# Performance work log

Measured on AMD Instinct MI355X. Metric: run time of the kernel, lower is better.

Reference implementation:

```python
import jax, jax.numpy as jnp
import numpy as np

NUM_EXPERTS = 8
TOP_K = 2
HIDDEN = 2048
INTER = 5632
TOKENS = 2048
W_SCALE = 0.02  # keep activations in a sane numeric range


def setup_inputs() -> dict:
    key = jax.random.key(0)
    k1, k2, k3, k4, k5 = jax.random.split(key, 5)
    hidden_states = jax.random.normal(k1, (TOKENS, HIDDEN), dtype=jnp.float32)
    router_logits = jax.random.normal(k2, (TOKENS, NUM_EXPERTS), dtype=jnp.float32)
    w1 = jax.random.normal(k3, (NUM_EXPERTS, INTER, HIDDEN), dtype=jnp.float32) * W_SCALE
    w3 = jax.random.normal(k4, (NUM_EXPERTS, INTER, HIDDEN), dtype=jnp.float32) * W_SCALE
    w2 = jax.random.normal(k5, (NUM_EXPERTS, HIDDEN, INTER), dtype=jnp.float32) * W_SCALE
    return {"hidden_states": hidden_states, "router_logits": router_logits,
            "w1": w1, "w3": w3, "w2": w2}


def reference(hidden_states, router_logits, w1, w3, w2):
    # Routing: top-k over softmax(logits), renormalized (standard TopK routing).
    T = hidden_states.shape[0]
    probs = jax.nn.softmax(router_logits.astype(jnp.float32), axis=-1)  # [T, E]
    top_w, top_idx = jax.lax.top_k(probs, TOP_K)                        # [T, K]
    top_w = top_w / jnp.sum(top_w, axis=-1, keepdims=True)
    # Per-token per-expert combine weight (0 for unselected experts): [T, E]
    comb = jnp.zeros((T, NUM_EXPERTS), dtype=jnp.float32)
    comb = comb.at[jnp.arange(T)[:, None], top_idx].add(top_w)
    x = hidden_states.astype(jnp.float32)  # accumulation in fp32 as in reference
    out = jnp.zeros_like(x)
    for e in range(NUM_EXPERTS):  # fixed small expert count; data dims vectorized
        gate = x @ w1[e].T                     # [T, I]
        up = x @ w3[e].T                       # [T, I]
        y = (jax.nn.silu(gate) * up) @ w2[e].T  # [T, H]
        out = out + comb[:, e:e + 1] * y
    return out
```

## Files before the change

kernel.cpp:

```cpp
#include <hip/hip_runtime.h>
#include <hip/hip_bf16.h>
#include <cstdint>
#include <cstddef>

#define NTOK 2048
#define HID  2048
#define NINT 5632
#define NEXP 8

typedef __attribute__((ext_vector_type(8))) short short8;
typedef __attribute__((ext_vector_type(4))) float f32x4;
typedef __attribute__((ext_vector_type(4))) int   int4v;
typedef __attribute__((ext_vector_type(4))) float fl4;

__device__ __forceinline__ unsigned short f2bf(float f) {
    union { float f; unsigned int u; } v; v.f = f;
    unsigned int r = (v.u + 0x7fffu + ((v.u >> 16) & 1u)) >> 16;
    return (unsigned short)r;
}

__global__ void zero_kernel(float* __restrict__ out, int* __restrict__ meta) {
    int idx = blockIdx.x * blockDim.x + threadIdx.x;
    fl4 z = {0.f, 0.f, 0.f, 0.f};
    ((fl4*)out)[idx] = z;
    if (blockIdx.x == 0 && threadIdx.x < 16) meta[threadIdx.x] = 0;
}

__device__ __forceinline__ void top2_route(const float* __restrict__ lg, int t,
                                           int& e0, int& e1, float& w0, float& w1) {
    float l[NEXP];
#pragma unroll
    for (int e = 0; e < NEXP; ++e) l[e] = lg[t * NEXP + e];
    e0 = 0; float b0l = l[0];
#pragma unroll
    for (int e = 1; e < NEXP; ++e) if (l[e] > b0l) { b0l = l[e]; e0 = e; }
    e1 = (e0 == 0) ? 1 : 0; float b1l = l[e1];
#pragma unroll
    for (int e = 0; e < NEXP; ++e) {
        if (e == e0) continue;
        if (l[e] > b1l) { b1l = l[e]; e1 = e; }
    }
    float m = b0l;
    float p0 = __expf(b0l - m), p1 = __expf(b1l - m);
    float inv = 1.f / (p0 + p1);
    w0 = p0 * inv; w1 = p1 * inv;
}

__global__ void route_count(const float* __restrict__ logits, int* __restrict__ meta) {
    int t = blockIdx.x * blockDim.x + threadIdx.x;
    int e0, e1; float w0, w1;
    top2_route(logits, t, e0, e1, w0, w1);
    atomicAdd(&meta[e0], 1);
    atomicAdd(&meta[e1], 1);
}

__global__ void scan_kernel(int* __restrict__ meta) {
    if (threadIdx.x == 0 && blockIdx.x == 0) {
        int s = 0;
#pragma unroll
        for (int e = 0; e < NEXP; ++e) { meta[16 + e] = s; s += meta[e]; }
        meta[16 + NEXP] = s;
    }
}

__global__ void route_assign(const float* __restrict__ logits, int* __restrict__ meta,
                             int* __restrict__ rowTok, float* __restrict__ rowW) {
    int t = blockIdx.x * blockDim.x + threadIdx.x;
    int e0, e1; float w0, w1;
    top2_route(logits, t, e0, e1, w0, w1);
    int p0 = atomicAdd(&meta[8 + e0], 1);
    int s0 = meta[16 + e0] + p0;
    rowTok[s0] = t; rowW[s0] = w0;
    int p1 = atomicAdd(&meta[8 + e1], 1);
    int s1 = meta[16 + e1] + p1;
    rowTok[s1] = t; rowW[s1] = w1;
}

__global__ void gather_x(const float* __restrict__ x, const int* __restrict__ rowTok,
                         unsigned short* __restrict__ xg) {
    int slot = blockIdx.x;
    int tok = rowTok[slot];
    int c = threadIdx.x;
    const fl4* src = (const fl4*)(x + (size_t)tok * HID);
    fl4 a = src[c * 2], b = src[c * 2 + 1];
    short8 v;
    v[0] = (short)f2bf(a[0]); v[1] = (short)f2bf(a[1]); v[2] = (short)f2bf(a[2]); v[3] = (short)f2bf(a[3]);
    v[4] = (short)f2bf(b[0]); v[5] = (short)f2bf(b[1]); v[6] = (short)f2bf(b[2]); v[7] = (short)f2bf(b[3]);
    *(short8*)(xg + (size_t)slot * HID + c * 8) = v;
}

__global__ __launch_bounds__(512, 2) void gemm1_kernel(
        const unsigned short* __restrict__ xg,
        const float* __restrict__ w1, const float* __restrict__ w3,
        const int* __restrict__ meta, unsigned short* __restrict__ act) {
    int it = blockIdx.x;
    int e  = blockIdx.y;
    int ch = blockIdx.z;
    int r0 = meta[16 + e];
    int Ne = meta[16 + e + 1] - r0;
    int cb = ch * 256;
    if (cb >= Ne) return;

    __shared__ __align__(16) short As[256][72];
    __shared__ __align__(16) short Bs[128][72];

    int tid = threadIdx.x;
    int lane = tid & 63, w = tid >> 6;

    f32x4 acc[2][8];
#pragma unroll
    for (int m = 0; m < 2; ++m)
#pragma unroll
        for (int n = 0; n < 8; ++n) acc[m][n] = (f32x4){0.f, 0.f, 0.f, 0.f};

    int ar = tid >> 1, ah = (tid & 1) * 32;
    int asrow = cb + ar;
    const unsigned short* aptr = xg + (size_t)(r0 + (asrow < Ne ? asrow : 0)) * HID + ah;
    int br = tid >> 2, bq = (tid & 3) * 16;
    const float* wsrc = (br < 64)
        ? (w1 + ((size_t)e * NINT + (size_t)it * 64 + br) * HID + bq)
        : (w3 + ((size_t)e * NINT + (size_t)it * 64 + (br - 64)) * HID + bq);

    for (int k0 = 0; k0 < HID; k0 += 64) {
        int4v av[4];
#pragma unroll
        for (int i = 0; i < 4; ++i) av[i] = *(const int4v*)(aptr + k0 + i * 8);
        fl4 bv[4];
#pragma unroll
        for (int i = 0; i < 4; ++i) bv[i] = *(const fl4*)(wsrc + k0 + i * 4);
        short8 c0, c1;
#pragma unroll
        for (int i = 0; i < 4; ++i) { c0[i] = (short)f2bf(bv[0][i]); c0[i + 4] = (short)f2bf(bv[1][i]); }
#pragma unroll
        for (int i = 0; i < 4; ++i) { c1[i] = (short)f2bf(bv[2][i]); c1[i + 4] = (short)f2bf(bv[3][i]); }

#pragma unroll
        for (int i = 0; i < 4; ++i) *(int4v*)&As[ar][ah + i * 8] = av[i];
        *(short8*)&Bs[br][bq] = c0;
        *(short8*)&Bs[br][bq + 8] = c1;
        __syncthreads();

#pragma unroll
        for (int kk = 0; kk < 64; kk += 32) {
            int ko = kk + (lane >> 4) * 8;
            short8 a0 = *(const short8*)&As[w * 32 + (lane & 15)][ko];
            short8 a1 = *(const short8*)&As[w * 32 + 16 + (lane & 15)][ko];
#pragma unroll
            for (int n = 0; n < 8; ++n) {
                short8 b = *(const short8*)&Bs[n * 16 + (lane & 15)][ko];
                acc[0][n] = __builtin_amdgcn_mfma_f32_16x16x32_bf16(a0, b, acc[0][n], 0, 0, 0);
                acc[1][n] = __builtin_amdgcn_mfma_f32_16x16x32_bf16(a1, b, acc[1][n], 0, 0, 0);
            }
        }
        __syncthreads();
    }

    int rq = lane >> 4, cl = lane & 15;
#pragma unroll
    for (int m = 0; m < 2; ++m) {
#pragma unroll
        for (int n = 0; n < 4; ++n) {
            f32x4 g = acc[m][n], u = acc[m][n + 4];
#pragma unroll
            for (int j = 0; j < 4; ++j) {
                int lr = w * 32 + m * 16 + rq * 4 + j;
                int srow = cb + lr;
                if (srow < Ne) {
                    float gv = g[j];
                    float y = gv / (1.f + __expf(-gv)) * u[j];
                    act[(size_t)(r0 + srow) * NINT + it * 64 + n * 16 + cl] = f2bf(y);
                }
            }
        }
    }
}

__global__ __launch_bounds__(512, 2) void gemm2_kernel(
        const unsigned short* __restrict__ act, const float* __restrict__ w2,
        const int* __restrict__ meta, const int* __restrict__ rowTok,
        const float* __restrict__ rowW, float* __restrict__ out) {
    int ht = blockIdx.x;
    int e  = blockIdx.y;
    int ch = blockIdx.z;
    int r0 = meta[16 + e];
    int Ne = meta[16 + e + 1] - r0;
    int cb = ch * 256;
    if (cb >= Ne) return;

    __shared__ __align__(16) short As[256][72];
    __shared__ __align__(16) short Bs[64][72];

    int tid = threadIdx.x;
    int lane = tid & 63, w = tid >> 6;

    f32x4 acc[2][4];
#pragma unroll
    for (int m = 0; m < 2; ++m)
#pragma unroll
        for (int n = 0; n < 4; ++n) acc[m][n] = (f32x4){0.f, 0.f, 0.f, 0.f};

    int ar = tid >> 1, ah = (tid & 1) * 32;
    int asrow = cb + ar;
    const unsigned short* aptr = act + (size_t)(r0 + (asrow < Ne ? asrow : 0)) * NINT + ah;
    int br = tid >> 3, bq = (tid & 7) * 8;
    const float* bptr = w2 + ((size_t)e * HID + (size_t)ht * 64 + br) * NINT + bq;

    for (int k0 = 0; k0 < NINT; k0 += 64) {
        int4v av[4];
#pragma unroll
        for (int i = 0; i < 4; ++i) av[i] = *(const int4v*)(aptr + k0 + i * 8);
        fl4 bv0 = *(const fl4*)(bptr + k0);
        fl4 bv1 = *(const fl4*)(bptr + k0 + 4);
        short8 bc;
#pragma unroll
        for (int i = 0; i < 4; ++i) { bc[i] = (short)f2bf(bv0[i]); bc[i + 4] = (short)f2bf(bv1[i]); }

#pragma unroll
        for (int i = 0; i < 4; ++i) *(int4v*)&As[ar][ah + i * 8] = av[i];
        *(short8*)&Bs[br][bq] = bc;
        __syncthreads();

#pragma unroll
        for (int kk = 0; kk < 64; kk += 32) {
            int ko = kk + (lane >> 4) * 8;
            short8 a0 = *(const short8*)&As[w * 32 + (lane & 15)][ko];
            short8 a1 = *(const short8*)&As[w * 32 + 16 + (lane & 15)][ko];
#pragma unroll
            for (int n = 0; n < 4; ++n) {
                short8 b = *(const short8*)&Bs[n * 16 + (lane & 15)][ko];
                acc[0][n] = __builtin_amdgcn_mfma_f32_16x16x32_bf16(a0, b, acc[0][n], 0, 0, 0);
                acc[1][n] = __builtin_amdgcn_mfma_f32_16x16x32_bf16(a1, b, acc[1][n], 0, 0, 0);
            }
        }
        __syncthreads();
    }

    int rq = lane >> 4, cl = lane & 15;
#pragma unroll
    for (int m = 0; m < 2; ++m) {
#pragma unroll
        for (int j = 0; j < 4; ++j) {
            int lr = w * 32 + m * 16 + rq * 4 + j;
            int srow = cb + lr;
            if (srow < Ne) {
                int slot = r0 + srow;
                int tok = rowTok[slot];
                float sw = rowW[slot];
#pragma unroll
                for (int n = 0; n < 4; ++n) {
                    atomicAdd(&out[(size_t)tok * HID + ht * 64 + n * 16 + cl], acc[m][n][j] * sw);
                }
            }
        }
    }
}

extern "C" void kernel_launch(void* const* d_in, const int* in_sizes, int n_in,
                              void* d_out, int out_size, void* d_ws, size_t ws_size,
                              hipStream_t stream) {
    const float* x      = (const float*)d_in[0];
    const float* logits = (const float*)d_in[1];
    const float* w1     = (const float*)d_in[2];
    const float* w3     = (const float*)d_in[3];
    const float* w2     = (const float*)d_in[4];
    float* out = (float*)d_out;

    char* ws = (char*)d_ws;
    int*   meta   = (int*)ws;
    int*   rowTok = (int*)(ws + 512);
    float* rowW   = (float*)(ws + 512 + 16384);
    unsigned short* xg  = (unsigned short*)(ws + (1u << 20));
    unsigned short* act = (unsigned short*)(ws + (18u << 20));

    zero_kernel<<<4096, 256, 0, stream>>>(out, meta);
    route_count<<<8, 256, 0, stream>>>(logits, meta);
    scan_kernel<<<1, 1, 0, stream>>>(meta);
    route_assign<<<8, 256, 0, stream>>>(logits, meta, rowTok, rowW);
    gather_x<<<4096, 256, 0, stream>>>(x, rowTok, xg);
    gemm1_kernel<<<dim3(88, 8, 8), 512, 0, stream>>>(xg, w1, w3, meta, act);
    gemm2_kernel<<<dim3(32, 8, 8), 512, 0, stream>>>(act, w2, meta, rowTok, rowW, out);
}
```

Baseline: 741.3 us.

## Register double-buffer global loads in both GEMMs and halve gemm1 N-tile

Both expert GEMMs now prefetch the next K-slice of activations and fp32 weights into registers while the current slice is in shared memory and feeding MFMAs, hiding global load latency behind compute. Gemm1's intermediate tile shrinks from 64 to 32 columns per block (doubling the grid to 176 tiles), which reduces accumulator registers and shared memory per block. The trade-off is more blocks re-reading the same gathered activation rows, and extra registers held for the prefetch buffers.

```diff
diff --git a/kernel.cpp b/kernel.cpp
--- a/kernel.cpp
+++ b/kernel.cpp
@@ -102,65 +102,68 @@
     if (cb >= Ne) return;
 
     __shared__ __align__(16) short As[256][72];
-    __shared__ __align__(16) short Bs[128][72];
+    __shared__ __align__(16) short Bs[64][72];
 
     int tid = threadIdx.x;
     int lane = tid & 63, w = tid >> 6;
 
-    f32x4 acc[2][8];
+    f32x4 acc[2][4];
 #pragma unroll
     for (int m = 0; m < 2; ++m)
 #pragma unroll
-        for (int n = 0; n < 8; ++n) acc[m][n] = (f32x4){0.f, 0.f, 0.f, 0.f};
+        for (int n = 0; n < 4; ++n) acc[m][n] = (f32x4){0.f, 0.f, 0.f, 0.f};
 
     int ar = tid >> 1, ah = (tid & 1) * 32;
     int asrow = cb + ar;
     const unsigned short* aptr = xg + (size_t)(r0 + (asrow < Ne ? asrow : 0)) * HID + ah;
-    int br = tid >> 2, bq = (tid & 3) * 16;
-    const float* wsrc = (br < 64)
-        ? (w1 + ((size_t)e * NINT + (size_t)it * 64 + br) * HID + bq)
-        : (w3 + ((size_t)e * NINT + (size_t)it * 64 + (br - 64)) * HID + bq);
-
-    for (int k0 = 0; k0 < HID; k0 += 64) {
-        int4v av[4];
-#pragma unroll
-        for (int i = 0; i < 4; ++i) av[i] = *(const int4v*)(aptr + k0 + i * 8);
-        fl4 bv[4];
-#pragma unroll
-        for (int i = 0; i < 4; ++i) bv[i] = *(const fl4*)(wsrc + k0 + i * 4);
-        short8 c0, c1;
-#pragma unroll
-        for (int i = 0; i < 4; ++i) { c0[i] = (short)f2bf(bv[0][i]); c0[i + 4] = (short)f2bf(bv[1][i]); }
-#pragma unroll
-        for (int i = 0; i < 4; ++i) { c1[i] = (short)f2bf(bv[2][i]); c1[i + 4] = (short)f2bf(bv[3][i]); }
-
-#pragma unroll
-        for (int i = 0; i < 4; ++i) *(int4v*)&As[ar][ah + i * 8] = av[i];
-        *(short8*)&Bs[br][bq] = c0;
-        *(short8*)&Bs[br][bq + 8] = c1;
-        __syncthreads();
-
-#pragma unroll
-        for (int kk = 0; kk < 64; kk += 32) {
-            int ko = kk + (lane >> 4) * 8;
-            short8 a0 = *(const short8*)&As[w * 32 + (lane & 15)][ko];
-            short8 a1 = *(const short8*)&As[w * 32 + 16 + (lane & 15)][ko];
-#pragma unroll
-            for (int n = 0; n < 8; ++n) {
-                short8 b = *(const short8*)&Bs[n * 16 + (lane & 15)][ko];
-                acc[0][n] = __builtin_amdgcn_mfma_f32_16x16x32_bf16(a0, b, acc[0][n], 0, 0, 0);
-                acc[1][n] = __builtin_amdgcn_mfma_f32_16x16x32_bf16(a1, b, acc[1][n], 0, 0, 0);
-            }
-        }
-        __syncthreads();
-    }
+    int br = tid >> 3, bq = (tid & 7) * 8;
+    const float* wsrc = (br < 32)
+        ? (w1 + ((size_t)e * NINT + (size_t)it * 32 + br) * HID + bq)
+        : (w3 + ((size_t)e * NINT + (size_t)it * 32 + (br - 32)) * HID + bq);
+
+    int4v ra[2][4];
+    fl4   rb[2][2];
+
+#define G1_LOAD(S, K0) do { \
+        _Pragma("unroll") for (int i = 0; i < 4; ++i) ra[S][i] = *(const int4v*)(aptr + (K0) + i * 8); \
+        _Pragma("unroll") for (int i = 0; i < 2; ++i) rb[S][i] = *(const fl4*)(wsrc + (K0) + i * 4); \
+    } while (0)
+
+#define G1_SC(S) do { \
+        short8 bc; \
+        _Pragma("unroll") for (int i = 0; i < 4; ++i) { \
+            bc[i] = (short)f2bf(rb[S][0][i]); bc[i + 4] = (short)f2bf(rb[S][1][i]); } \
+        __syncthreads(); \
+        _Pragma("unroll") for (int i = 0; i < 4; ++i) *(int4v*)&As[ar][ah + i * 8] = ra[S][i]; \
+        *(short8*)&Bs[br][bq] = bc; \
+        __syncthreads(); \
+        _Pragma("unroll") for (int kk = 0; kk < 64; kk += 32) { \
+            int ko = kk + (lane >> 4) * 8; \
+            short8 a0 = *(const short8*)&As[w * 32 + (lane & 15)][ko]; \
+            short8 a1 = *(const short8*)&As[w * 32 + 16 + (lane & 15)][ko]; \
+            _Pragma("unroll") for (int n = 0; n < 4; ++n) { \
+                short8 b = *(const short8*)&Bs[n * 16 + (lane & 15)][ko]; \
+                acc[0][n] = __builtin_amdgcn_mfma_f32_16x16x32_bf16(a0, b, acc[0][n], 0, 0, 0); \
+                acc[1][n] = __builtin_amdgcn_mfma_f32_16x16x32_bf16(a1, b, acc[1][n], 0, 0, 0); } } \
+    } while (0)
+
+    G1_LOAD(0, 0);
+#pragma unroll 1
+    for (int k0 = 0; k0 < HID; k0 += 128) {
+        G1_LOAD(1, k0 + 64);
+        G1_SC(0);
+        if (k0 + 128 < HID) G1_LOAD(0, k0 + 128);
+        G1_SC(1);
+    }
+#undef G1_LOAD
+#undef G1_SC
 
     int rq = lane >> 4, cl = lane & 15;
 #pragma unroll
     for (int m = 0; m < 2; ++m) {
 #pragma unroll
-        for (int n = 0; n < 4; ++n) {
-            f32x4 g = acc[m][n], u = acc[m][n + 4];
+        for (int n = 0; n < 2; ++n) {
+            f32x4 g = acc[m][n], u = acc[m][n + 2];
 #pragma unroll
             for (int j = 0; j < 4; ++j) {
                 int lr = w * 32 + m * 16 + rq * 4 + j;
@@ -168,7 +171,7 @@
                 if (srow < Ne) {
                     float gv = g[j];
                     float y = gv / (1.f + __expf(-gv)) * u[j];
-                    act[(size_t)(r0 + srow) * NINT + it * 64 + n * 16 + cl] = f2bf(y);
+                    act[(size_t)(r0 + srow) * NINT + it * 32 + n * 16 + cl] = f2bf(y);
                 }
             }
         }
@@ -205,35 +208,42 @@
     int br = tid >> 3, bq = (tid & 7) * 8;
     const float* bptr = w2 + ((size_t)e * HID + (size_t)ht * 64 + br) * NINT + bq;
 
-    for (int k0 = 0; k0 < NINT; k0 += 64) {
-        int4v av[4];
-#pragma unroll
-        for (int i = 0; i < 4; ++i) av[i] = *(const int4v*)(aptr + k0 + i * 8);
-        fl4 bv0 = *(const fl4*)(bptr + k0);
-        fl4 bv1 = *(const fl4*)(bptr + k0 + 4);
-        short8 bc;
-#pragma unroll
-        for (int i = 0; i < 4; ++i) { bc[i] = (short)f2bf(bv0[i]); bc[i + 4] = (short)f2bf(bv1[i]); }
-
-#pragma unroll
-        for (int i = 0; i < 4; ++i) *(int4v*)&As[ar][ah + i * 8] = av[i];
-        *(short8*)&Bs[br][bq] = bc;
-        __syncthreads();
-
-#pragma unroll
-        for (int kk = 0; kk < 64; kk += 32) {
-            int ko = kk + (lane >> 4) * 8;
-            short8 a0 = *(const short8*)&As[w * 32 + (lane & 15)][ko];
-            short8 a1 = *(const short8*)&As[w * 32 + 16 + (lane & 15)][ko];
-#pragma unroll
-            for (int n = 0; n < 4; ++n) {
-                short8 b = *(const short8*)&Bs[n * 16 + (lane & 15)][ko];
-                acc[0][n] = __builtin_amdgcn_mfma_f32_16x16x32_bf16(a0, b, acc[0][n], 0, 0, 0);
-                acc[1][n] = __builtin_amdgcn_mfma_f32_16x16x32_bf16(a1, b, acc[1][n], 0, 0, 0);
-            }
-        }
-        __syncthreads();
-    }
+    int4v ra[2][4];
+    fl4   rb[2][2];
+
+#define G2_LOAD(S, K0) do { \
+        _Pragma("unroll") for (int i = 0; i < 4; ++i) ra[S][i] = *(const int4v*)(aptr + (K0) + i * 8); \
+        _Pragma("unroll") for (int i = 0; i < 2; ++i) rb[S][i] = *(const fl4*)(bptr + (K0) + i * 4); \
+    } while (0)
+
+#define G2_SC(S) do { \
+        short8 bc; \
+        _Pragma("unroll") for (int i = 0; i < 4; ++i) { \
+            bc[i] = (short)f2bf(rb[S][0][i]); bc[i + 4] = (short)f2bf(rb[S][1][i]); } \
+        __syncthreads(); \
+        _Pragma("unroll") for (int i = 0; i < 4; ++i) *(int4v*)&As[ar][ah + i * 8] = ra[S][i]; \
+        *(short8*)&Bs[br][bq] = bc; \
+        __syncthreads(); \
+        _Pragma("unroll") for (int kk = 0; kk < 64; kk += 32) { \
+            int ko = kk + (lane >> 4) * 8; \
+            short8 a0 = *(const short8*)&As[w * 32 + (lane & 15)][ko]; \
+            short8 a1 = *(const short8*)&As[w * 32 + 16 + (lane & 15)][ko]; \
+            _Pragma("unroll") for (int n = 0; n < 4; ++n) { \
+                short8 b = *(const short8*)&Bs[n * 16 + (lane & 15)][ko]; \
+                acc[0][n] = __builtin_amdgcn_mfma_f32_16x16x32_bf16(a0, b, acc[0][n], 0, 0, 0); \
+                acc[1][n] = __builtin_amdgcn_mfma_f32_16x16x32_bf16(a1, b, acc[1][n], 0, 0, 0); } } \
+    } while (0)
+
+    G2_LOAD(0, 0);
+#pragma unroll 1
+    for (int k0 = 0; k0 < NINT; k0 += 128) {
+        G2_LOAD(1, k0 + 64);
+        G2_SC(0);
+        if (k0 + 128 < NINT) G2_LOAD(0, k0 + 128);
+        G2_SC(1);
+    }
+#undef G2_LOAD
+#undef G2_SC
 
     int rq = lane >> 4, cl = lane & 15;
 #pragma unroll
@@ -277,6 +287,6 @@
     scan_kernel<<<1, 1, 0, stream>>>(meta);
     route_assign<<<8, 256, 0, stream>>>(logits, meta, rowTok, rowW);
     gather_x<<<4096, 256, 0, stream>>>(x, rowTok, xg);
-    gemm1_kernel<<<dim3(88, 8, 8), 512, 0, stream>>>(xg, w1, w3, meta, act);
+    gemm1_kernel<<<dim3(176, 8, 8), 512, 0, stream>>>(xg, w1, w3, meta, act);
     gemm2_kernel<<<dim3(32, 8, 8), 512, 0, stream>>>(act, w2, meta, rowTok, rowW, out);
 }
```

Result: slower. 931.8 us (+25.7%).

## Drop LDS staging in MoE GEMMs, load MFMA operands directly with register prefetch

Applied to the files above, without the earlier changes.

Both expert GEMMs stop staging tiles through shared memory. Each wave now loads its A and B MFMA fragments straight from global memory into registers and prefetches the next k-step while the current one computes. Blocks cover 128-row chunks assigned through a compact list across experts (find_chunk), replacing the padded 3D grid of mostly early-exiting blocks. gemm2 also widens its N tile to 128. This removes LDS traffic and __syncthreads, and fewer launched blocks do nothing. In exchange, weights are re-read from global memory by every wave rather than shared across the block, which leans on L2 hit rates and uncoalesced row-strided loads.

```diff
diff --git a/kernel.cpp b/kernel.cpp
--- a/kernel.cpp
+++ b/kernel.cpp
@@ -10,7 +10,6 @@
 
 typedef __attribute__((ext_vector_type(8))) short short8;
 typedef __attribute__((ext_vector_type(4))) float f32x4;
-typedef __attribute__((ext_vector_type(4))) int   int4v;
 typedef __attribute__((ext_vector_type(4))) float fl4;
 
 __device__ __forceinline__ unsigned short f2bf(float f) {
@@ -89,167 +88,159 @@
     *(short8*)(xg + (size_t)slot * HID + c * 8) = v;
 }
 
-__global__ __launch_bounds__(512, 2) void gemm1_kernel(
+__device__ __forceinline__ bool find_chunk(const int* __restrict__ meta, int yc,
+                                           int& e, int& ch, int& r0, int& Ne) {
+    e = -1; ch = 0; int accb = 0;
+#pragma unroll
+    for (int i = 0; i < NEXP; ++i) {
+        int nei = meta[17 + i] - meta[16 + i];
+        int cnt = (nei + 127) >> 7;
+        if (e < 0 && yc < accb + cnt) { e = i; ch = yc - accb; }
+        accb += cnt;
+    }
+    if (e < 0) return false;
+    r0 = meta[16 + e]; Ne = meta[17 + e] - r0;
+    return true;
+}
+
+__global__ __launch_bounds__(256, 2) void gemm1_kernel(
         const unsigned short* __restrict__ xg,
         const float* __restrict__ w1, const float* __restrict__ w3,
         const int* __restrict__ meta, unsigned short* __restrict__ act) {
     int it = blockIdx.x;
-    int e  = blockIdx.y;
-    int ch = blockIdx.z;
-    int r0 = meta[16 + e];
-    int Ne = meta[16 + e + 1] - r0;
-    int cb = ch * 256;
-    if (cb >= Ne) return;
-
-    __shared__ __align__(16) short As[256][72];
-    __shared__ __align__(16) short Bs[128][72];
-
-    int tid = threadIdx.x;
-    int lane = tid & 63, w = tid >> 6;
+    int e, ch, r0, Ne;
+    if (!find_chunk(meta, blockIdx.y, e, ch, r0, Ne)) return;
+
+    int lane = threadIdx.x & 63, w = threadIdx.x >> 6;
+    int cl = lane & 15, kq = lane >> 4;
+    int rowb = ch * 128 + w * 32;
+
+    int ra0 = rowb + cl;      if (ra0 > Ne - 1) ra0 = Ne - 1;
+    int ra1 = rowb + 16 + cl; if (ra1 > Ne - 1) ra1 = Ne - 1;
+    const unsigned short* a0p = xg + (size_t)(r0 + ra0) * HID + kq * 8;
+    const unsigned short* a1p = xg + (size_t)(r0 + ra1) * HID + kq * 8;
+
+    const float* bp[8];
+#pragma unroll
+    for (int f = 0; f < 4; ++f) {
+        bp[f]     = w1 + ((size_t)e * NINT + it * 64 + f * 16 + cl) * HID + kq * 8;
+        bp[f + 4] = w3 + ((size_t)e * NINT + it * 64 + f * 16 + cl) * HID + kq * 8;
+    }
 
     f32x4 acc[2][8];
 #pragma unroll
     for (int m = 0; m < 2; ++m)
 #pragma unroll
-        for (int n = 0; n < 8; ++n) acc[m][n] = (f32x4){0.f, 0.f, 0.f, 0.f};
-
-    int ar = tid >> 1, ah = (tid & 1) * 32;
-    int asrow = cb + ar;
-    const unsigned short* aptr = xg + (size_t)(r0 + (asrow < Ne ? asrow : 0)) * HID + ah;
-    int br = tid >> 2, bq = (tid & 3) * 16;
-    const float* wsrc = (br < 64)
-        ? (w1 + ((size_t)e * NINT + (size_t)it * 64 + br) * HID + bq)
-        : (w3 + ((size_t)e * NINT + (size_t)it * 64 + (br - 64)) * HID + bq);
-
-    for (int k0 = 0; k0 < HID; k0 += 64) {
-        int4v av[4];
-#pragma unroll
-        for (int i = 0; i < 4; ++i) av[i] = *(const int4v*)(aptr + k0 + i * 8);
-        fl4 bv[4];
-#pragma unroll
-        for (int i = 0; i < 4; ++i) bv[i] = *(const fl4*)(wsrc + k0 + i * 4);
-        short8 c0, c1;
-#pragma unroll
-        for (int i = 0; i < 4; ++i) { c0[i] = (short)f2bf(bv[0][i]); c0[i + 4] = (short)f2bf(bv[1][i]); }
-#pragma unroll
-        for (int i = 0; i < 4; ++i) { c1[i] = (short)f2bf(bv[2][i]); c1[i + 4] = (short)f2bf(bv[3][i]); }
-
-#pragma unroll
-        for (int i = 0; i < 4; ++i) *(int4v*)&As[ar][ah + i * 8] = av[i];
-        *(short8*)&Bs[br][bq] = c0;
-        *(short8*)&Bs[br][bq + 8] = c1;
-        __syncthreads();
-
-#pragma unroll
-        for (int kk = 0; kk < 64; kk += 32) {
-            int ko = kk + (lane >> 4) * 8;
-            short8 a0 = *(const short8*)&As[w * 32 + (lane & 15)][ko];
-            short8 a1 = *(const short8*)&As[w * 32 + 16 + (lane & 15)][ko];
-#pragma unroll
-            for (int n = 0; n < 8; ++n) {
-                short8 b = *(const short8*)&Bs[n * 16 + (lane & 15)][ko];
-                acc[0][n] = __builtin_amdgcn_mfma_f32_16x16x32_bf16(a0, b, acc[0][n], 0, 0, 0);
-                acc[1][n] = __builtin_amdgcn_mfma_f32_16x16x32_bf16(a1, b, acc[1][n], 0, 0, 0);
-            }
-        }
-        __syncthreads();
-    }
-
-    int rq = lane >> 4, cl = lane & 15;
+        for (int f = 0; f < 8; ++f) acc[m][f] = (f32x4){0.f, 0.f, 0.f, 0.f};
+
+    fl4 b0[8], b1[8];
+#pragma unroll
+    for (int f = 0; f < 8; ++f) { b0[f] = *(const fl4*)(bp[f]); b1[f] = *(const fl4*)(bp[f] + 4); }
+    short8 a0 = *(const short8*)a0p;
+    short8 a1 = *(const short8*)a1p;
+
+#pragma unroll 1
+    for (int k0 = 0; k0 < HID; k0 += 32) {
+        __builtin_amdgcn_s_barrier();
+        int kn = (k0 + 32 < HID) ? (k0 + 32) : 0;
+        short8 a0n = *(const short8*)(a0p + kn);
+        short8 a1n = *(const short8*)(a1p + kn);
+#pragma unroll
+        for (int f = 0; f < 8; ++f) {
+            short8 bb;
+#pragma unroll
+            for (int i = 0; i < 4; ++i) { bb[i] = (short)f2bf(b0[f][i]); bb[i + 4] = (short)f2bf(b1[f][i]); }
+            b0[f] = *(const fl4*)(bp[f] + kn);
+            b1[f] = *(const fl4*)(bp[f] + kn + 4);
+            acc[0][f] = __builtin_amdgcn_mfma_f32_16x16x32_bf16(a0, bb, acc[0][f], 0, 0, 0);
+            acc[1][f] = __builtin_amdgcn_mfma_f32_16x16x32_bf16(a1, bb, acc[1][f], 0, 0, 0);
+        }
+        a0 = a0n; a1 = a1n;
+    }
+
 #pragma unroll
     for (int m = 0; m < 2; ++m) {
 #pragma unroll
-        for (int n = 0; n < 4; ++n) {
-            f32x4 g = acc[m][n], u = acc[m][n + 4];
+        for (int f = 0; f < 4; ++f) {
+            f32x4 g = acc[m][f], u = acc[m][f + 4];
 #pragma unroll
             for (int j = 0; j < 4; ++j) {
-                int lr = w * 32 + m * 16 + rq * 4 + j;
-                int srow = cb + lr;
-                if (srow < Ne) {
+                int lr = rowb + m * 16 + kq * 4 + j;
+                if (lr < Ne) {
                     float gv = g[j];
                     float y = gv / (1.f + __expf(-gv)) * u[j];
-                    act[(size_t)(r0 + srow) * NINT + it * 64 + n * 16 + cl] = f2bf(y);
+                    act[(size_t)(r0 + lr) * NINT + it * 64 + f * 16 + cl] = f2bf(y);
                 }
             }
         }
     }
 }
 
-__global__ __launch_bounds__(512, 2) void gemm2_kernel(
+__global__ __launch_bounds__(256, 2) void gemm2_kernel(
         const unsigned short* __restrict__ act, const float* __restrict__ w2,
         const int* __restrict__ meta, const int* __restrict__ rowTok,
         const float* __restrict__ rowW, float* __restrict__ out) {
     int ht = blockIdx.x;
-    int e  = blockIdx.y;
-    int ch = blockIdx.z;
-    int r0 = meta[16 + e];
-    int Ne = meta[16 + e + 1] - r0;
-    int cb = ch * 256;
-    if (cb >= Ne) return;
-
-    __shared__ __align__(16) short As[256][72];
-    __shared__ __align__(16) short Bs[64][72];
-
-    int tid = threadIdx.x;
-    int lane = tid & 63, w = tid >> 6;
-
-    f32x4 acc[2][4];
+    int e, ch, r0, Ne;
+    if (!find_chunk(meta, blockIdx.y, e, ch, r0, Ne)) return;
+
+    int lane = threadIdx.x & 63, w = threadIdx.x >> 6;
+    int cl = lane & 15, kq = lane >> 4;
+    int rowb = ch * 128 + w * 32;
+
+    int ra0 = rowb + cl;      if (ra0 > Ne - 1) ra0 = Ne - 1;
+    int ra1 = rowb + 16 + cl; if (ra1 > Ne - 1) ra1 = Ne - 1;
+    const unsigned short* a0p = act + (size_t)(r0 + ra0) * NINT + kq * 8;
+    const unsigned short* a1p = act + (size_t)(r0 + ra1) * NINT + kq * 8;
+
+    const float* bp[8];
+#pragma unroll
+    for (int f = 0; f < 8; ++f)
+        bp[f] = w2 + ((size_t)e * HID + ht * 128 + f * 16 + cl) * NINT + kq * 8;
+
+    f32x4 acc[2][8];
 #pragma unroll
     for (int m = 0; m < 2; ++m)
 #pragma unroll
-        for (int n = 0; n < 4; ++n) acc[m][n] = (f32x4){0.f, 0.f, 0.f, 0.f};
-
-    int ar = tid >> 1, ah = (tid & 1) * 32;
-    int asrow = cb + ar;
-    const unsigned short* aptr = act + (size_t)(r0 + (asrow < Ne ? asrow : 0)) * NINT + ah;
-    int br = tid >> 3, bq = (tid & 7) * 8;
-    const float* bptr = w2 + ((size_t)e * HID + (size_t)ht * 64 + br) * NINT + bq;
-
-    for (int k0 = 0; k0 < NINT; k0 += 64) {
-        int4v av[4];
-#pragma unroll
-        for (int i = 0; i < 4; ++i) av[i] = *(const int4v*)(aptr + k0 + i * 8);
-        fl4 bv0 = *(const fl4*)(bptr + k0);
-        fl4 bv1 = *(const fl4*)(bptr + k0 + 4);
-        short8 bc;
-#pragma unroll
-        for (int i = 0; i < 4; ++i) { bc[i] = (short)f2bf(bv0[i]); bc[i + 4] = (short)f2bf(bv1[i]); }
-
-#pragma unroll
-        for (int i = 0; i < 4; ++i) *(int4v*)&As[ar][ah + i * 8] = av[i];
-        *(short8*)&Bs[br][bq] = bc;
-        __syncthreads();
-
-#pragma unroll
-        for (int kk = 0; kk < 64; kk += 32) {
-            int ko = kk + (lane >> 4) * 8;
-            short8 a0 = *(const short8*)&As[w * 32 + (lane & 15)][ko];
-            short8 a1 = *(const short8*)&As[w * 32 + 16 + (lane & 15)][ko];
-#pragma unroll
-            for (int n = 0; n < 4; ++n) {
-                short8 b = *(const short8*)&Bs[n * 16 + (lane & 15)][ko];
-                acc[0][n] = __builtin_amdgcn_mfma_f32_16x16x32_bf16(a0, b, acc[0][n], 0, 0, 0);
-                acc[1][n] = __builtin_amdgcn_mfma_f32_16x16x32_bf16(a1, b, acc[1][n], 0, 0, 0);
-            }
-        }
-        __syncthreads();
-    }
-
-    int rq = lane >> 4, cl = lane & 15;
+        for (int f = 0; f < 8; ++f) acc[m][f] = (f32x4){0.f, 0.f, 0.f, 0.f};
+
+    fl4 b0[8], b1[8];
+#pragma unroll
+    for (int f = 0; f < 8; ++f) { b0[f] = *(const fl4*)(bp[f]); b1[f] = *(const fl4*)(bp[f] + 4); }
+    short8 a0 = *(const short8*)a0p;
+    short8 a1 = *(const short8*)a1p;
+
+#pragma unroll 1
+    for (int k0 = 0; k0 < NINT; k0 += 32) {
+        __builtin_amdgcn_s_barrier();
+        int kn = (k0 + 32 < NINT) ? (k0 + 32) : 0;
+        short8 a0n = *(const short8*)(a0p + kn);
+        short8 a1n = *(const short8*)(a1p + kn);
+#pragma unroll
+        for (int f = 0; f < 8; ++f) {
+            short8 bb;
+#pragma unroll
+            for (int i = 0; i < 4; ++i) { bb[i] = (short)f2bf(b0[f][i]); bb[i + 4] = (short)f2bf(b1[f][i]); }
+            b0[f] = *(const fl4*)(bp[f] + kn);
+            b1[f] = *(const fl4*)(bp[f] + kn + 4);
+            acc[0][f] = __builtin_amdgcn_mfma_f32_16x16x32_bf16(a0, bb, acc[0][f], 0, 0, 0);
+            acc[1][f] = __builtin_amdgcn_mfma_f32_16x16x32_bf16(a1, bb, acc[1][f], 0, 0, 0);
+        }
+        a0 = a0n; a1 = a1n;
+    }
+
 #pragma unroll
     for (int m = 0; m < 2; ++m) {
 #pragma unroll
         for (int j = 0; j < 4; ++j) {
-            int lr = w * 32 + m * 16 + rq * 4 + j;
-            int srow = cb + lr;
-            if (srow < Ne) {
-                int slot = r0 + srow;
+            int lr = rowb + m * 16 + kq * 4 + j;
+            if (lr < Ne) {
+                int slot = r0 + lr;
                 int tok = rowTok[slot];
                 float sw = rowW[slot];
 #pragma unroll
-                for (int n = 0; n < 4; ++n) {
-                    atomicAdd(&out[(size_t)tok * HID + ht * 64 + n * 16 + cl], acc[m][n][j] * sw);
-                }
+                for (int f = 0; f < 8; ++f)
+                    atomicAdd(&out[(size_t)tok * HID + ht * 128 + f * 16 + cl], acc[m][f][j] * sw);
             }
         }
     }
@@ -277,6 +268,6 @@
     scan_kernel<<<1, 1, 0, stream>>>(meta);
     route_assign<<<8, 256, 0, stream>>>(logits, meta, rowTok, rowW);
     gather_x<<<4096, 256, 0, stream>>>(x, rowTok, xg);
-    gemm1_kernel<<<dim3(88, 8, 8), 512, 0, stream>>>(xg, w1, w3, meta, act);
-    gemm2_kernel<<<dim3(32, 8, 8), 512, 0, stream>>>(act, w2, meta, rowTok, rowW, out);
-}
+    gemm1_kernel<<<dim3(88, 40), 256, 0, stream>>>(xg, w1, w3, meta, act);
+    gemm2_kernel<<<dim3(16, 40), 256, 0, stream>>>(act, w2, meta, rowTok, rowW, out);
+}
```

New measurement: 2.853 ms. +284.9%, slower.

## Shrink GEMM tiles, swizzle LDS, reorder grid for weight reuse

Applied to the files above, without the earlier changes.

Both expert GEMMs now use 256-thread blocks with 128-row token tiles and narrower weight tiles (32 intermediate columns for gate/up, 32 hidden columns for down). The grid is reordered so token chunks vary fastest, letting blocks that share a weight tile run together and reuse it from cache. LDS uses an XOR swizzle instead of padding to avoid bank conflicts, the fp32-to-bf16 conversion uses packed intrinsics, and the register-staged loads are issued before the first barrier. The smaller tiles aim for more blocks and better occupancy, but they lower MFMA work per LDS load and double the fp32 weight reads per output.

```diff
diff --git a/kernel.cpp b/kernel.cpp
--- a/kernel.cpp
+++ b/kernel.cpp
@@ -11,12 +11,19 @@
 typedef __attribute__((ext_vector_type(8))) short short8;
 typedef __attribute__((ext_vector_type(4))) float f32x4;
 typedef __attribute__((ext_vector_type(4))) int   int4v;
+typedef __attribute__((ext_vector_type(2))) unsigned int uint2v;
 typedef __attribute__((ext_vector_type(4))) float fl4;
 
 __device__ __forceinline__ unsigned short f2bf(float f) {
     union { float f; unsigned int u; } v; v.f = f;
     unsigned int r = (v.u + 0x7fffu + ((v.u >> 16) & 1u)) >> 16;
     return (unsigned short)r;
+}
+
+__device__ __forceinline__ unsigned int pk2(float x, float y) {
+    __hip_bfloat162 h = __float22bfloat162_rn(make_float2(x, y));
+    union { __hip_bfloat162 h; unsigned int u; } c; c.h = h;
+    return c.u;
 }
 
 __global__ void zero_kernel(float* __restrict__ out, int* __restrict__ meta) {
@@ -89,167 +96,199 @@
     *(short8*)(xg + (size_t)slot * HID + c * 8) = v;
 }
 
-__global__ __launch_bounds__(512, 2) void gemm1_kernel(
+__global__ __launch_bounds__(256, 4) void gemm1_kernel(
         const unsigned short* __restrict__ xg,
         const float* __restrict__ w1, const float* __restrict__ w3,
         const int* __restrict__ meta, unsigned short* __restrict__ act) {
-    int it = blockIdx.x;
-    int e  = blockIdx.y;
-    int ch = blockIdx.z;
-    int r0 = meta[16 + e];
-    int Ne = meta[16 + e + 1] - r0;
-    int cb = ch * 256;
+    const int ch = blockIdx.x;
+    const int it = blockIdx.y;
+    const int e  = blockIdx.z;
+    const int r0 = meta[16 + e];
+    const int Ne = meta[17 + e] - r0;
+    const int cb = ch * 128;
     if (cb >= Ne) return;
 
-    __shared__ __align__(16) short As[256][72];
-    __shared__ __align__(16) short Bs[128][72];
-
-    int tid = threadIdx.x;
-    int lane = tid & 63, w = tid >> 6;
-
-    f32x4 acc[2][8];
-#pragma unroll
-    for (int m = 0; m < 2; ++m)
-#pragma unroll
-        for (int n = 0; n < 8; ++n) acc[m][n] = (f32x4){0.f, 0.f, 0.f, 0.f};
-
-    int ar = tid >> 1, ah = (tid & 1) * 32;
-    int asrow = cb + ar;
-    const unsigned short* aptr = xg + (size_t)(r0 + (asrow < Ne ? asrow : 0)) * HID + ah;
-    int br = tid >> 2, bq = (tid & 3) * 16;
-    const float* wsrc = (br < 64)
-        ? (w1 + ((size_t)e * NINT + (size_t)it * 64 + br) * HID + bq)
-        : (w3 + ((size_t)e * NINT + (size_t)it * 64 + (br - 64)) * HID + bq);
-
+    __shared__ __align__(16) short As[128][64];
+    __shared__ __align__(16) short Bs[64][64];
+
+    const int tid = threadIdx.x;
+    const int wv = tid >> 6, l = tid & 63;
+    const int cl = l & 15, kq = l >> 4;
+
+    const unsigned short* agp[4];
+    short* awr[4];
+    {
+        const int slot = tid & 7;
+#pragma unroll
+        for (int j = 0; j < 4; ++j) {
+            int row = (tid >> 3) + j * 32;
+            int gr = cb + row; if (gr > Ne - 1) gr = Ne - 1;
+            agp[j] = xg + (size_t)(r0 + gr) * HID + slot * 8;
+            awr[j] = &As[row][(slot ^ (row & 7)) * 8];
+        }
+    }
+    const int brow = tid >> 2, bq = tid & 3;
+    const float* bgp = ((brow < 32)
+        ? (w1 + ((size_t)e * NINT + (size_t)it * 32 + brow) * HID)
+        : (w3 + ((size_t)e * NINT + (size_t)it * 32 + (brow - 32)) * HID)) + bq * 4;
+    unsigned int* bwr[4];
+#pragma unroll
+    for (int j2 = 0; j2 < 4; ++j2) {
+        int s = 2 * j2 + (bq >> 1);
+        bwr[j2] = (unsigned int*)&Bs[brow][(s ^ (brow & 7)) * 8 + (bq & 1) * 4];
+    }
+
+    f32x4 acc[2][4];
+#pragma unroll
+    for (int rf = 0; rf < 2; ++rf)
+#pragma unroll
+        for (int cf = 0; cf < 4; ++cf) acc[rf][cf] = (f32x4){0.f, 0.f, 0.f, 0.f};
+
+#pragma unroll 1
     for (int k0 = 0; k0 < HID; k0 += 64) {
-        int4v av[4];
-#pragma unroll
-        for (int i = 0; i < 4; ++i) av[i] = *(const int4v*)(aptr + k0 + i * 8);
-        fl4 bv[4];
-#pragma unroll
-        for (int i = 0; i < 4; ++i) bv[i] = *(const fl4*)(wsrc + k0 + i * 4);
-        short8 c0, c1;
-#pragma unroll
-        for (int i = 0; i < 4; ++i) { c0[i] = (short)f2bf(bv[0][i]); c0[i + 4] = (short)f2bf(bv[1][i]); }
-#pragma unroll
-        for (int i = 0; i < 4; ++i) { c1[i] = (short)f2bf(bv[2][i]); c1[i + 4] = (short)f2bf(bv[3][i]); }
-
-#pragma unroll
-        for (int i = 0; i < 4; ++i) *(int4v*)&As[ar][ah + i * 8] = av[i];
-        *(short8*)&Bs[br][bq] = c0;
-        *(short8*)&Bs[br][bq + 8] = c1;
+        int4v ra[4];
+#pragma unroll
+        for (int j = 0; j < 4; ++j) ra[j] = *(const int4v*)(agp[j] + k0);
+        fl4 rb[4];
+#pragma unroll
+        for (int j2 = 0; j2 < 4; ++j2) rb[j2] = *(const fl4*)(bgp + k0 + 16 * j2);
+        uint2v bw[4];
+#pragma unroll
+        for (int j2 = 0; j2 < 4; ++j2) {
+            bw[j2][0] = pk2(rb[j2][0], rb[j2][1]);
+            bw[j2][1] = pk2(rb[j2][2], rb[j2][3]);
+        }
         __syncthreads();
-
-#pragma unroll
-        for (int kk = 0; kk < 64; kk += 32) {
-            int ko = kk + (lane >> 4) * 8;
-            short8 a0 = *(const short8*)&As[w * 32 + (lane & 15)][ko];
-            short8 a1 = *(const short8*)&As[w * 32 + 16 + (lane & 15)][ko];
-#pragma unroll
-            for (int n = 0; n < 8; ++n) {
-                short8 b = *(const short8*)&Bs[n * 16 + (lane & 15)][ko];
-                acc[0][n] = __builtin_amdgcn_mfma_f32_16x16x32_bf16(a0, b, acc[0][n], 0, 0, 0);
-                acc[1][n] = __builtin_amdgcn_mfma_f32_16x16x32_bf16(a1, b, acc[1][n], 0, 0, 0);
+#pragma unroll
+        for (int j = 0; j < 4; ++j) *(int4v*)awr[j] = ra[j];
+#pragma unroll
+        for (int j2 = 0; j2 < 4; ++j2) *(uint2v*)bwr[j2] = bw[j2];
+        __syncthreads();
+#pragma unroll
+        for (int kk = 0; kk < 2; ++kk) {
+            const int sx = ((kk * 4 + kq) ^ (cl & 7)) * 8;
+            short8 af0 = *(const short8*)&As[wv * 32 + cl][sx];
+            short8 af1 = *(const short8*)&As[wv * 32 + 16 + cl][sx];
+#pragma unroll
+            for (int cf = 0; cf < 4; ++cf) {
+                short8 bfm = *(const short8*)&Bs[cf * 16 + cl][sx];
+                acc[0][cf] = __builtin_amdgcn_mfma_f32_16x16x32_bf16(af0, bfm, acc[0][cf], 0, 0, 0);
+                acc[1][cf] = __builtin_amdgcn_mfma_f32_16x16x32_bf16(af1, bfm, acc[1][cf], 0, 0, 0);
             }
         }
-        __syncthreads();
-    }
-
-    int rq = lane >> 4, cl = lane & 15;
-#pragma unroll
-    for (int m = 0; m < 2; ++m) {
-#pragma unroll
-        for (int n = 0; n < 4; ++n) {
-            f32x4 g = acc[m][n], u = acc[m][n + 4];
+    }
+
+#pragma unroll
+    for (int rf = 0; rf < 2; ++rf) {
+#pragma unroll
+        for (int cf = 0; cf < 2; ++cf) {
+            f32x4 g = acc[rf][cf], u = acc[rf][cf + 2];
 #pragma unroll
             for (int j = 0; j < 4; ++j) {
-                int lr = w * 32 + m * 16 + rq * 4 + j;
-                int srow = cb + lr;
-                if (srow < Ne) {
+                int r = cb + wv * 32 + rf * 16 + kq * 4 + j;
+                if (r < Ne) {
                     float gv = g[j];
                     float y = gv / (1.f + __expf(-gv)) * u[j];
-                    act[(size_t)(r0 + srow) * NINT + it * 64 + n * 16 + cl] = f2bf(y);
+                    act[(size_t)(r0 + r) * NINT + (size_t)it * 32 + cf * 16 + cl] = f2bf(y);
                 }
             }
         }
     }
 }
 
-__global__ __launch_bounds__(512, 2) void gemm2_kernel(
+__global__ __launch_bounds__(256, 4) void gemm2_kernel(
         const unsigned short* __restrict__ act, const float* __restrict__ w2,
         const int* __restrict__ meta, const int* __restrict__ rowTok,
         const float* __restrict__ rowW, float* __restrict__ out) {
-    int ht = blockIdx.x;
-    int e  = blockIdx.y;
-    int ch = blockIdx.z;
-    int r0 = meta[16 + e];
-    int Ne = meta[16 + e + 1] - r0;
-    int cb = ch * 256;
+    const int ch = blockIdx.x;
+    const int ht = blockIdx.y;
+    const int e  = blockIdx.z;
+    const int r0 = meta[16 + e];
+    const int Ne = meta[17 + e] - r0;
+    const int cb = ch * 128;
     if (cb >= Ne) return;
 
-    __shared__ __align__(16) short As[256][72];
-    __shared__ __align__(16) short Bs[64][72];
-
-    int tid = threadIdx.x;
-    int lane = tid & 63, w = tid >> 6;
-
-    f32x4 acc[2][4];
-#pragma unroll
-    for (int m = 0; m < 2; ++m)
-#pragma unroll
-        for (int n = 0; n < 4; ++n) acc[m][n] = (f32x4){0.f, 0.f, 0.f, 0.f};
-
-    int ar = tid >> 1, ah = (tid & 1) * 32;
-    int asrow = cb + ar;
-    const unsigned short* aptr = act + (size_t)(r0 + (asrow < Ne ? asrow : 0)) * NINT + ah;
-    int br = tid >> 3, bq = (tid & 7) * 8;
-    const float* bptr = w2 + ((size_t)e * HID + (size_t)ht * 64 + br) * NINT + bq;
-
+    __shared__ __align__(16) short As[128][64];
+    __shared__ __align__(16) short Bs[32][64];
+
+    const int tid = threadIdx.x;
+    const int wv = tid >> 6, l = tid & 63;
+    const int cl = l & 15, kq = l >> 4;
+
+    const unsigned short* agp[4];
+    short* awr[4];
+    {
+        const int slot = tid & 7;
+#pragma unroll
+        for (int j = 0; j < 4; ++j) {
+            int row = (tid >> 3) + j * 32;
+            int gr = cb + row; if (gr > Ne - 1) gr = Ne - 1;
+            agp[j] = act + (size_t)(r0 + gr) * NINT + slot * 8;
+            awr[j] = &As[row][(slot ^ (row & 7)) * 8];
+        }
+    }
+    const int brow = tid >> 3, bq = tid & 7;
+    const float* bgp = w2 + ((size_t)e * HID + (size_t)ht * 32 + brow) * NINT + bq * 4;
+    unsigned int* bwr[2];
+#pragma unroll
+    for (int j2 = 0; j2 < 2; ++j2) {
+        int s = 4 * j2 + (bq >> 1);
+        bwr[j2] = (unsigned int*)&Bs[brow][(s ^ (brow & 7)) * 8 + (bq & 1) * 4];
+    }
+
+    f32x4 acc[2][2];
+#pragma unroll
+    for (int rf = 0; rf < 2; ++rf)
+#pragma unroll
+        for (int cf = 0; cf < 2; ++cf) acc[rf][cf] = (f32x4){0.f, 0.f, 0.f, 0.f};
+
+#pragma unroll 1
     for (int k0 = 0; k0 < NINT; k0 += 64) {
-        int4v av[4];
-#pragma unroll
-        for (int i = 0; i < 4; ++i) av[i] = *(const int4v*)(aptr + k0 + i * 8);
-        fl4 bv0 = *(const fl4*)(bptr + k0);
-        fl4 bv1 = *(const fl4*)(bptr + k0 + 4);
-        short8 bc;
-#pragma unroll
-        for (int i = 0; i < 4; ++i) { bc[i] = (short)f2bf(bv0[i]); bc[i + 4] = (short)f2bf(bv1[i]); }
-
-#pragma unroll
-        for (int i = 0; i < 4; ++i) *(int4v*)&As[ar][ah + i * 8] = av[i];
-        *(short8*)&Bs[br][bq] = bc;
+        int4v ra[4];
+#pragma unroll
+        for (int j = 0; j < 4; ++j) ra[j] = *(const int4v*)(agp[j] + k0);
+        fl4 rb[2];
+#pragma unroll
+        for (int j2 = 0; j2 < 2; ++j2) rb[j2] = *(const fl4*)(bgp + k0 + 32 * j2);
+        uint2v bw[2];
+#pragma unroll
+        for (int j2 = 0; j2 < 2; ++j2) {
+            bw[j2][0] = pk2(rb[j2][0], rb[j2][1]);
+            bw[j2][1] = pk2(rb[j2][2], rb[j2][3]);
+        }
         __syncthreads();
-
-#pragma unroll
-        for (int kk = 0; kk < 64; kk += 32) {
-            int ko = kk + (lane >> 4) * 8;
-            short8 a0 = *(const short8*)&As[w * 32 + (lane & 15)][ko];
-            short8 a1 = *(const short8*)&As[w * 32 + 16 + (lane & 15)][ko];
-#pragma unroll
-            for (int n = 0; n < 4; ++n) {
-                short8 b = *(const short8*)&Bs[n * 16 + (lane & 15)][ko];
-                acc[0][n] = __builtin_amdgcn_mfma_f32_16x16x32_bf16(a0, b, acc[0][n], 0, 0, 0);
-                acc[1][n] = __builtin_amdgcn_mfma_f32_16x16x32_bf16(a1, b, acc[1][n], 0, 0, 0);
+#pragma unroll
+        for (int j = 0; j < 4; ++j) *(int4v*)awr[j] = ra[j];
+#pragma unroll
+        for (int j2 = 0; j2 < 2; ++j2) *(uint2v*)bwr[j2] = bw[j2];
+        __syncthreads();
+#pragma unroll
+        for (int kk = 0; kk < 2; ++kk) {
+            const int sx = ((kk * 4 + kq) ^ (cl & 7)) * 8;
+            short8 af0 = *(const short8*)&As[wv * 32 + cl][sx];
+            short8 af1 = *(const short8*)&As[wv * 32 + 16 + cl][sx];
+#pragma unroll
+            for (int cf = 0; cf < 2; ++cf) {
+                short8 bfm = *(const short8*)&Bs[cf * 16 + cl][sx];
+                acc[0][cf] = __builtin_amdgcn_mfma_f32_16x16x32_bf16(af0, bfm, acc[0][cf], 0, 0, 0);
+                acc[1][cf] = __builtin_amdgcn_mfma_f32_16x16x32_bf16(af1, bfm, acc[1][cf], 0, 0, 0);
             }
         }
-        __syncthreads();
-    }
-
-    int rq = lane >> 4, cl = lane & 15;
-#pragma unroll
-    for (int m = 0; m < 2; ++m) {
+    }
+
+#pragma unroll
+    for (int rf = 0; rf < 2; ++rf) {
 #pragma unroll
         for (int j = 0; j < 4; ++j) {
-            int lr = w * 32 + m * 16 + rq * 4 + j;
-            int srow = cb + lr;
-            if (srow < Ne) {
-                int slot = r0 + srow;
+            int r = cb + wv * 32 + rf * 16 + kq * 4 + j;
+            if (r < Ne) {
+                int slot = r0 + r;
                 int tok = rowTok[slot];
                 float sw = rowW[slot];
 #pragma unroll
-                for (int n = 0; n < 4; ++n) {
-                    atomicAdd(&out[(size_t)tok * HID + ht * 64 + n * 16 + cl], acc[m][n][j] * sw);
-                }
+                for (int cf = 0; cf < 2; ++cf)
+                    atomicAdd(&out[(size_t)tok * HID + (size_t)ht * 32 + cf * 16 + cl],
+                              acc[rf][cf][j] * sw);
             }
         }
     }
@@ -277,6 +316,6 @@
     scan_kernel<<<1, 1, 0, stream>>>(meta);
     route_assign<<<8, 256, 0, stream>>>(logits, meta, rowTok, rowW);
     gather_x<<<4096, 256, 0, stream>>>(x, rowTok, xg);
-    gemm1_kernel<<<dim3(88, 8, 8), 512, 0, stream>>>(xg, w1, w3, meta, act);
-    gemm2_kernel<<<dim3(32, 8, 8), 512, 0, stream>>>(act, w2, meta, rowTok, rowW, out);
-}
+    gemm1_kernel<<<dim3(16, 176, 8), 256, 0, stream>>>(xg, w1, w3, meta, act);
+    gemm2_kernel<<<dim3(16, 64, 8), 256, 0, stream>>>(act, w2, meta, rowTok, rowW, out);
+}
```

Result: slower. 2.121 ms (+186.1%).
